# Kernel optimization log

Hardware: AMD Instinct MI355X
Metric: run time of the kernel (lower is better)

The kernel has to match this reference:

```python
import jax, jax.numpy as jnp
import numpy as np

EMB = 768
HEADS = 12
DH = EMB // HEADS


def setup_inputs() -> dict:
    key = jax.random.key(0)
    k = jax.random.split(key, 5)
    s = 0.02
    return {
        "x": jax.random.normal(k[0], (4, 2048, EMB), dtype=jnp.float32),
        "qkv_w": jax.random.normal(k[1], (3 * EMB, EMB), dtype=jnp.float32) * s,  # torch Linear weight [out,in]
        "qkv_b": jax.random.normal(k[2], (3 * EMB,), dtype=jnp.float32) * s,
        "proj_w": jax.random.normal(k[3], (EMB, EMB), dtype=jnp.float32) * s,
        "proj_b": jax.random.normal(k[4], (EMB,), dtype=jnp.float32) * s,
    }


def reference(x, qkv_w, qkv_b, proj_w, proj_b):
    b, n, _ = x.shape
    qkv = x @ qkv_w.T + qkv_b  # [b, n, 3*EMB]
    # rearrange 'b n (h d qkv) -> qkv b h n d'
    qkv = qkv.reshape(b, n, HEADS, DH, 3)
    qkv = jnp.transpose(qkv, (4, 0, 2, 1, 3))  # [3, b, h, n, d]
    q, k, v = qkv[0], qkv[1], qkv[2]
    e = jnp.einsum("bhqd,bhkd->bhqk", q, k)
    scale = jnp.float32(EMB) ** 0.5
    # NOTE: original divides by sqrt(emb_size) AFTER softmax (faithful to source)
    attn = jax.nn.softmax(e, axis=-1) / scale
    out = jnp.einsum("bhqk,bhkd->bhqd", attn, v)
    out = jnp.transpose(out, (0, 2, 1, 3)).reshape(b, n, EMB)  # 'b h n d -> b n (h d)'
    return out @ proj_w.T + proj_b
```

## Files before the change

kernel.cpp:

```cpp
#include <hip/hip_runtime.h>
#include <hip/hip_bf16.h>

typedef unsigned short ushort_t;
typedef __attribute__((ext_vector_type(8))) short s16x8;
typedef __attribute__((ext_vector_type(4))) float f32x4;
typedef __attribute__((ext_vector_type(16))) float f32x16;
typedef __attribute__((ext_vector_type(4))) unsigned int u32x4;

#define EMB 768
#define HEADS 12
#define DH 64
#define BATCH 4
#define SEQ 2048
#define MTOK (BATCH*SEQ)
#define NQKV (3*EMB)
#define LOG2E 1.44269504088896f

__device__ __forceinline__ ushort_t f2bf(float f) {
  unsigned u = __float_as_uint(f);
  u += 0x7fffu + ((u >> 16) & 1u);
  return (ushort_t)(u >> 16);
}
__device__ __forceinline__ unsigned pk2bf(float a, float b) {
  return (unsigned)f2bf(a) | ((unsigned)f2bf(b) << 16);
}
__device__ __forceinline__ unsigned cvtpk(float lo, float hi_) {
  unsigned d;
  asm("v_cvt_pk_bf16_f32 %0, %1, %2" : "=v"(d) : "v"(lo), "v"(hi_));
  return d;
}

__device__ __forceinline__ void gload_lds16(const void* g, void* l) {
  __builtin_amdgcn_global_load_lds(
      (const __attribute__((address_space(1))) unsigned*)g,
      (__attribute__((address_space(3))) unsigned*)l, 16, 0, 0);
}

__global__ void cvt_bf16(const float* __restrict__ in, ushort_t* __restrict__ out, int n4) {
  int i = blockIdx.x * blockDim.x + threadIdx.x;
  if (i >= n4) return;
  const float4 v = reinterpret_cast<const float4*>(in)[i];
  reinterpret_cast<uint2*>(out)[i] = make_uint2(pk2bf(v.x, v.y), pk2bf(v.z, v.w));
}

#define TM 128
#define TN 128
#define BKG 64

template<int MODE>
__global__ __launch_bounds__(256, 2) void gemm_bt(
    const ushort_t* __restrict__ A, const ushort_t* __restrict__ BT,
    const float* __restrict__ bias, float* __restrict__ Cf,
    ushort_t* __restrict__ Qd, ushort_t* __restrict__ Kd, ushort_t* __restrict__ Vt,
    int M, int N, int K)
{
  __shared__ alignas(16) ushort_t As[TM*BKG];
  __shared__ alignas(16) ushort_t Bs[TN*BKG];
  const int t = threadIdx.x;
  const int w = t >> 6, l = t & 63, g = l >> 4, r = l & 15;
  const int wr = w >> 1, wc = w & 1;
  const int m0 = blockIdx.y * TM, n0 = blockIdx.x * TN;

  f32x4 acc[4][4] = {};

  for (int kt = 0; kt < K; kt += BKG) {
#pragma unroll
    for (int p = 0; p < 4; ++p) {
      const int off = (t + p*256) * 16;
      const int row = off >> 7;
      const int scb = (off & 127) ^ ((row & 7) << 4);
      gload_lds16(A  + (size_t)(m0+row)*K + kt + (scb>>1), (char*)As + off);
      gload_lds16(BT + (size_t)(n0+row)*K + kt + (scb>>1), (char*)Bs + off);
    }
    __syncthreads();

    s16x8 fa[4][2], fb[4][2];
#pragma unroll
    for (int mi = 0; mi < 4; ++mi)
#pragma unroll
      for (int kk = 0; kk < 2; ++kk) {
        const int ra = wr*64 + mi*16 + r;
        fa[mi][kk] = *(const s16x8*)((const char*)As + ra*128 + ((g*16 + kk*64) ^ ((ra&7)<<4)));
        const int rb = wc*64 + mi*16 + r;
        fb[mi][kk] = *(const s16x8*)((const char*)Bs + rb*128 + ((g*16 + kk*64) ^ ((rb&7)<<4)));
      }
#pragma unroll
    for (int mi = 0; mi < 4; ++mi)
#pragma unroll
      for (int ni = 0; ni < 4; ++ni) {
        acc[mi][ni] = __builtin_amdgcn_mfma_f32_16x16x32_bf16(fa[mi][0], fb[ni][0], acc[mi][ni], 0,0,0);
        acc[mi][ni] = __builtin_amdgcn_mfma_f32_16x16x32_bf16(fa[mi][1], fb[ni][1], acc[mi][ni], 0,0,0);
      }
    __syncthreads();
  }

#pragma unroll
  for (int ni = 0; ni < 4; ++ni) {
    const int col = n0 + wc*64 + ni*16 + r;
    const float bv = bias[col];
    int h_ = 0, d_ = 0, which = 0;
    if (MODE == 1) {
      h_ = col / 192;
      const int rem = col - h_*192;
      d_ = rem / 3;
      which = rem - d_*3;
    }
#pragma unroll
    for (int mi = 0; mi < 4; ++mi) {
#pragma unroll
      for (int q = 0; q < 4; ++q) {
        const int rowg = m0 + wr*64 + mi*16 + g*4 + q;
        const float v = acc[mi][ni][q] + bv;
        if (MODE == 0) {
          Cf[(size_t)rowg * N + col] = v;
        } else {
          const int bb = rowg >> 11, nn = rowg & 2047;
          if (which == 2) {
            const int np = (nn & ~12) | ((nn & 4) << 1) | ((nn & 8) >> 1);
            Vt[((size_t)(bb*HEADS + h_)*DH + d_)*SEQ + np] = f2bf(v);
          } else {
            const size_t idx = ((size_t)(bb*HEADS + h_)*SEQ + nn)*DH + d_;
            if (which == 0) Qd[idx] = f2bf(v * LOG2E);
            else            Kd[idx] = f2bf(v);
          }
        }
      }
    }
  }
}

#define NTIL 32

__global__ __launch_bounds__(256, 3) void attn_fwd(
    const ushort_t* __restrict__ Qd, const ushort_t* __restrict__ Kd,
    const ushort_t* __restrict__ Vt, ushort_t* __restrict__ Oa)
{
  __shared__ alignas(16) char L[3][16384];
  char* Lc = &L[0][0];

  const int t = threadIdx.x;
  const int w = t >> 6, l = t & 63;
  const int c31 = l & 31, hi = l >> 5;
  const int blk = blockIdx.x;
  const int logical = (blk & 7) * 96 + (blk >> 3);
  const int bh = logical >> 4;
  const int qt = logical & 15;
  const int q0 = qt * 128 + w * 32;
  const int b = bh / HEADS, h = bh - b * HEADS;

  const ushort_t* Qp = Qd + (size_t)bh * SEQ * DH;
  const ushort_t* Kp = Kd + (size_t)bh * SEQ * DH;
  const ushort_t* Vp = Vt + (size_t)bh * DH * SEQ;

  s16x8 qf[4];
  {
    const ushort_t* qp = Qp + (size_t)(q0 + c31) * DH + hi * 8;
#pragma unroll
    for (int c = 0; c < 4; ++c) qf[c] = *(const s16x8*)(qp + c * 16);
  }

  f32x16 oacc0 = {}, oacc1 = {};
  float ps0 = 0.f, ps1 = 0.f, ps2 = 0.f, ps3 = 0.f;

  const int ldsb = hi * 1024 + c31 * 16;
  const ushort_t* ksrc0 = Kp + (size_t)l * DH + w * 16;
  const ushort_t* vsrc0 = Vp + (size_t)l * SEQ + w * 16;
  char* kdst0 = Lc + w * 2048 + l * 16;

#define STAGE(bufc, tile_)                                                         \
  {                                                                                \
    const int tl = (tile_);                                                        \
    const ushort_t* ks = ksrc0 + (size_t)tl * (64 * DH);                           \
    const ushort_t* vs = vsrc0 + tl * 64;                                          \
    char* kd = kdst0 + (bufc) * 16384;                                             \
    gload_lds16(ks,     kd);                                                       \
    gload_lds16(ks + 8, kd + 1024);                                                \
    gload_lds16(vs,     kd + 8192);                                                \
    gload_lds16(vs + 8, kd + 9216);                                                \
  }

#define KGROUP(bufc, kg)                                                           \
  {                                                                                \
    const char* base = Lc + (bufc) * 16384 + ldsb;                                 \
    s16x8 kf0 = *(const s16x8*)(base + ((kg)*512 + 0*2048));                       \
    s16x8 kf1 = *(const s16x8*)(base + ((kg)*512 + 1*2048));                       \
    s16x8 kf2 = *(const s16x8*)(base + ((kg)*512 + 2*2048));                       \
    s16x8 kf3 = *(const s16x8*)(base + ((kg)*512 + 3*2048));                       \
    s16x8 va00 = *(const s16x8*)(base + (8192 + (kg)*4096 + 0*2048 + 0*512));      \
    s16x8 va01 = *(const s16x8*)(base + (8192 + (kg)*4096 + 1*2048 + 0*512));      \
    s16x8 va10 = *(const s16x8*)(base + (8192 + (kg)*4096 + 0*2048 + 1*512));      \
    s16x8 va11 = *(const s16x8*)(base + (8192 + (kg)*4096 + 1*2048 + 1*512));      \
    __builtin_amdgcn_s_setprio(1);                                                 \
    f32x16 s = {};                                                                 \
    s = __builtin_amdgcn_mfma_f32_32x32x16_bf16(kf0, qf[0], s, 0, 0, 0);           \
    s = __builtin_amdgcn_mfma_f32_32x32x16_bf16(kf1, qf[1], s, 0, 0, 0);           \
    s = __builtin_amdgcn_mfma_f32_32x32x16_bf16(kf2, qf[2], s, 0, 0, 0);           \
    s = __builtin_amdgcn_mfma_f32_32x32x16_bf16(kf3, qf[3], s, 0, 0, 0);           \
    __builtin_amdgcn_s_setprio(0);                                                 \
    float pe[16];                                                                  \
    _Pragma("unroll")                                                              \
    for (int r2 = 0; r2 < 16; ++r2) pe[r2] = __builtin_amdgcn_exp2f(s[r2]);        \
    ps0 += (pe[0]  + pe[1])  + (pe[2]  + pe[3]);                                   \
    ps1 += (pe[4]  + pe[5])  + (pe[6]  + pe[7]);                                   \
    ps2 += (pe[8]  + pe[9])  + (pe[10] + pe[11]);                                  \
    ps3 += (pe[12] + pe[13]) + (pe[14] + pe[15]);                                  \
    u32x4 f0u = { cvtpk(pe[0],  pe[1]),  cvtpk(pe[2],  pe[3]),                     \
                  cvtpk(pe[4],  pe[5]),  cvtpk(pe[6],  pe[7]) };                   \
    u32x4 f1u = { cvtpk(pe[8],  pe[9]),  cvtpk(pe[10], pe[11]),                    \
                  cvtpk(pe[12], pe[13]), cvtpk(pe[14], pe[15]) };                  \
    const s16x8 pf0 = __builtin_bit_cast(s16x8, f0u);                              \
    const s16x8 pf1 = __builtin_bit_cast(s16x8, f1u);                              \
    __builtin_amdgcn_s_setprio(1);                                                 \
    oacc0 = __builtin_amdgcn_mfma_f32_32x32x16_bf16(va00, pf0, oacc0, 0, 0, 0);    \
    oacc0 = __builtin_amdgcn_mfma_f32_32x32x16_bf16(va01, pf1, oacc0, 0, 0, 0);    \
    oacc1 = __builtin_amdgcn_mfma_f32_32x32x16_bf16(va10, pf0, oacc1, 0, 0, 0);    \
    oacc1 = __builtin_amdgcn_mfma_f32_32x32x16_bf16(va11, pf1, oacc1, 0, 0, 0);    \
    __builtin_amdgcn_s_setprio(0);                                                 \
  }

#define ITER(bufcur, bufn2, tt)                                                    \
  {                                                                                \
    asm volatile("s_barrier" ::: "memory");                                        \
    const int nt2 = (tt) + 2 < NTIL ? (tt) + 2 : NTIL - 1;                         \
    STAGE(bufn2, nt2);                                                             \
    asm volatile("s_waitcnt vmcnt(8)" ::: "memory");                               \
    asm volatile("s_barrier" ::: "memory");                                        \
    KGROUP(bufcur, 0);                                                             \
    KGROUP(bufcur, 1);                                                             \
  }

  STAGE(0, 0);
  STAGE(1, 1);
  for (int tt = 0; tt < NTIL - 2; tt += 3) {
    ITER(0, 2, tt);
    ITER(1, 0, tt + 1);
    ITER(2, 1, tt + 2);
  }
  ITER(0, 2, 30);
  ITER(1, 0, 31);
#undef ITER
#undef KGROUP
#undef STAGE

  const float psum = (ps0 + ps1) + (ps2 + ps3);
  const float lt = psum + __shfl_xor(psum, 32);
  const float scale = 0.036084391824351615f / lt;

  ushort_t* op = Oa + ((size_t)(b * SEQ + q0 + c31)) * EMB + h * DH;
#pragma unroll
  for (int f = 0; f < 2; ++f) {
    const f32x16& o = f ? oacc1 : oacc0;
#pragma unroll
    for (int rq = 0; rq < 4; ++rq) {
      const int dbase = f * 32 + 8 * rq + 4 * hi;
      uint2 u;
      u.x = pk2bf(o[rq*4+0] * scale, o[rq*4+1] * scale);
      u.y = pk2bf(o[rq*4+2] * scale, o[rq*4+3] * scale);
      *reinterpret_cast<uint2*>(op + dbase) = u;
    }
  }
}

extern "C" void kernel_launch(void* const* d_in, const int* in_sizes, int n_in,
                              void* d_out, int out_size, void* d_ws, size_t ws_size,
                              hipStream_t stream) {
  const float* x      = (const float*)d_in[0];
  const float* qkv_w  = (const float*)d_in[1];
  const float* qkv_b  = (const float*)d_in[2];
  const float* proj_w = (const float*)d_in[3];
  const float* proj_b = (const float*)d_in[4];
  float* out = (float*)d_out;

  ushort_t* xb    = (ushort_t*)d_ws;
  ushort_t* wqkv  = xb    + (size_t)MTOK*EMB;
  ushort_t* wproj = wqkv  + (size_t)NQKV*EMB;
  ushort_t* Qd    = wproj + (size_t)EMB*EMB;
  ushort_t* Kd    = Qd    + (size_t)MTOK*EMB;
  ushort_t* Vt    = Kd    + (size_t)MTOK*EMB;
  ushort_t* Oa    = Vt    + (size_t)MTOK*EMB;

  {
    int n4 = MTOK*EMB/4;
    cvt_bf16<<<(n4+255)/256, 256, 0, stream>>>(x, xb, n4);
  }
  {
    int n4 = NQKV*EMB/4;
    cvt_bf16<<<(n4+255)/256, 256, 0, stream>>>(qkv_w, wqkv, n4);
  }
  {
    int n4 = EMB*EMB/4;
    cvt_bf16<<<(n4+255)/256, 256, 0, stream>>>(proj_w, wproj, n4);
  }

  gemm_bt<1><<<dim3(NQKV/TN, MTOK/TM), 256, 0, stream>>>(
      xb, wqkv, qkv_b, nullptr, Qd, Kd, Vt, MTOK, NQKV, EMB);

  attn_fwd<<<768, 256, 0, stream>>>(Qd, Kd, Vt, Oa);

  gemm_bt<0><<<dim3(EMB/TN, MTOK/TM), 256, 0, stream>>>(
      Oa, wproj, proj_b, out, nullptr, nullptr, nullptr, MTOK, EMB, EMB);
}
```

Before: 164.8 us.

## Permute QKV weight rows so epilogue writes contiguous heads and vectorized V stores

```diff
diff --git a/kernel.cpp b/kernel.cpp
--- a/kernel.cpp
+++ b/kernel.cpp
@@ -41,6 +41,23 @@
   if (i >= n4) return;
   const float4 v = reinterpret_cast<const float4*>(in)[i];
   reinterpret_cast<uint2*>(out)[i] = make_uint2(pk2bf(v.x, v.y), pk2bf(v.z, v.w));
+}
+
+__global__ void cvt_wqkv(const float* __restrict__ w, const float* __restrict__ bias,
+                         ushort_t* __restrict__ out, float* __restrict__ bias_p, int n4) {
+  int i = blockIdx.x * blockDim.x + threadIdx.x;
+  if (i >= n4) return;
+  const int srcrow = i / 192;
+  const int c4 = i - srcrow * 192;
+  const int h = srcrow / 192;
+  const int rem = srcrow - h * 192;
+  const int d = rem / 3;
+  const int which = rem - d * 3;
+  const int dstrow = which * 768 + h * 64 + d;
+  const float4 v = reinterpret_cast<const float4*>(w)[i];
+  reinterpret_cast<uint2*>(out)[dstrow * 192 + c4] =
+      make_uint2(pk2bf(v.x, v.y), pk2bf(v.z, v.w));
+  if (c4 == 0) bias_p[dstrow] = bias[srcrow];
 }
 
 #define TM 128
@@ -59,7 +76,10 @@
   const int t = threadIdx.x;
   const int w = t >> 6, l = t & 63, g = l >> 4, r = l & 15;
   const int wr = w >> 1, wc = w & 1;
-  const int m0 = blockIdx.y * TM, n0 = blockIdx.x * TN;
+  int lin = blockIdx.y * gridDim.x + blockIdx.x;
+  const int cpx = (gridDim.x * gridDim.y) >> 3;
+  lin = (lin & 7) * cpx + (lin >> 3);
+  const int m0 = (lin / gridDim.x) * TM, n0 = (lin - (lin / gridDim.x) * gridDim.x) * TN;
 
   f32x4 acc[4][4] = {};
 
@@ -98,32 +118,41 @@
   for (int ni = 0; ni < 4; ++ni) {
     const int col = n0 + wc*64 + ni*16 + r;
     const float bv = bias[col];
-    int h_ = 0, d_ = 0, which = 0;
-    if (MODE == 1) {
-      h_ = col / 192;
-      const int rem = col - h_*192;
-      d_ = rem / 3;
-      which = rem - d_*3;
-    }
-#pragma unroll
-    for (int mi = 0; mi < 4; ++mi) {
-#pragma unroll
-      for (int q = 0; q < 4; ++q) {
-        const int rowg = m0 + wr*64 + mi*16 + g*4 + q;
-        const float v = acc[mi][ni][q] + bv;
-        if (MODE == 0) {
-          Cf[(size_t)rowg * N + col] = v;
-        } else {
-          const int bb = rowg >> 11, nn = rowg & 2047;
-          if (which == 2) {
-            const int np = (nn & ~12) | ((nn & 4) << 1) | ((nn & 8) >> 1);
-            Vt[((size_t)(bb*HEADS + h_)*DH + d_)*SEQ + np] = f2bf(v);
-          } else {
-            const size_t idx = ((size_t)(bb*HEADS + h_)*SEQ + nn)*DH + d_;
-            if (which == 0) Qd[idx] = f2bf(v * LOG2E);
-            else            Kd[idx] = f2bf(v);
+    if (MODE == 0) {
+#pragma unroll
+      for (int mi = 0; mi < 4; ++mi)
+#pragma unroll
+        for (int q = 0; q < 4; ++q) {
+          const int rowg = m0 + wr*64 + mi*16 + g*4 + q;
+          Cf[(size_t)rowg * N + col] = acc[mi][ni][q] + bv;
+        }
+    } else {
+      const int which = col / 768;
+      const int h_ = (col - which * 768) >> 6;
+      const int d_ = col & 63;
+      if (which == 2) {
+#pragma unroll
+        for (int mi = 0; mi < 4; ++mi) {
+          const int nn0 = m0 + wr*64 + mi*16 + g*4;
+          const int bb = nn0 >> 11, nl = nn0 & 2047;
+          const int np0 = (nl & ~12) | ((nl & 4) << 1) | ((nl & 8) >> 1);
+          uint2 u;
+          u.x = pk2bf(acc[mi][ni][0] + bv, acc[mi][ni][1] + bv);
+          u.y = pk2bf(acc[mi][ni][2] + bv, acc[mi][ni][3] + bv);
+          *reinterpret_cast<uint2*>(Vt + ((size_t)(bb*HEADS + h_)*DH + d_)*SEQ + np0) = u;
+        }
+      } else {
+        ushort_t* dst = (which == 0) ? Qd : Kd;
+        const float sc = (which == 0) ? LOG2E : 1.0f;
+#pragma unroll
+        for (int mi = 0; mi < 4; ++mi)
+#pragma unroll
+          for (int q = 0; q < 4; ++q) {
+            const int rowg = m0 + wr*64 + mi*16 + g*4 + q;
+            const int bb = rowg >> 11, nn = rowg & 2047;
+            dst[((size_t)(bb*HEADS + h_)*SEQ + nn)*DH + d_] =
+                f2bf((acc[mi][ni][q] + bv) * sc);
           }
-        }
       }
     }
   }
@@ -278,6 +307,7 @@
   ushort_t* Kd    = Qd    + (size_t)MTOK*EMB;
   ushort_t* Vt    = Kd    + (size_t)MTOK*EMB;
   ushort_t* Oa    = Vt    + (size_t)MTOK*EMB;
+  float*    biasp = (float*)(Oa + (size_t)MTOK*EMB);
 
   {
     int n4 = MTOK*EMB/4;
@@ -285,7 +315,7 @@
   }
   {
     int n4 = NQKV*EMB/4;
-    cvt_bf16<<<(n4+255)/256, 256, 0, stream>>>(qkv_w, wqkv, n4);
+    cvt_wqkv<<<(n4+255)/256, 256, 0, stream>>>(qkv_w, qkv_b, wqkv, biasp, n4);
   }
   {
     int n4 = EMB*EMB/4;
@@ -293,7 +323,7 @@
   }
 
   gemm_bt<1><<<dim3(NQKV/TN, MTOK/TM), 256, 0, stream>>>(
-      xb, wqkv, qkv_b, nullptr, Qd, Kd, Vt, MTOK, NQKV, EMB);
+      xb, wqkv, biasp, nullptr, Qd, Kd, Vt, MTOK, NQKV, EMB);
 
   attn_fwd<<<768, 256, 0, stream>>>(Qd, Kd, Vt, Oa);
 
```

Result: faster. 145.8 us (-11.5%).
